# Optimization experiments

Measured on AMD Instinct MI355X. Metric: run time of the kernel, lower is better.

## Reference

```python
import jax, jax.numpy as jnp
import numpy as np

D_MODEL = 1024
D_STATE = 16
D_CONV = 4
EXPAND = 2
NUM_LAYERS = 2
SEQ = 1024
BATCH = 2
D_INNER = EXPAND * D_MODEL          # 2048
DT_RANK = (D_MODEL + 15) // 16      # 64 (math.ceil(d_model/16))


def setup_inputs() -> dict:
    key = jax.random.key(0)
    ks = jax.random.split(key, 10)
    s = 0.02
    # A initialized as in mamba_ssm: A = repeat(arange(1, d_state+1), d_inner) -> A_log = log(A)
    A_log = jnp.log(jnp.broadcast_to(
        jnp.arange(1, D_STATE + 1, dtype=jnp.float32), (NUM_LAYERS, D_INNER, D_STATE)))
    return {
        "pe": jax.random.normal(ks[0], (SEQ, D_MODEL), jnp.float32) * s,
        "condition": jax.random.normal(ks[1], (BATCH, SEQ, D_MODEL), jnp.float32),
        "W_in": jax.random.normal(ks[2], (NUM_LAYERS, 2 * D_INNER, D_MODEL), jnp.float32) * s,
        "conv_w": jax.random.normal(ks[3], (NUM_LAYERS, D_INNER, D_CONV), jnp.float32) * s,
        "conv_b": jnp.zeros((NUM_LAYERS, D_INNER), jnp.float32),
        "W_x": jax.random.normal(ks[4], (NUM_LAYERS, DT_RANK + 2 * D_STATE, D_INNER), jnp.float32) * s,
        "W_dt": jax.random.normal(ks[5], (NUM_LAYERS, D_INNER, DT_RANK), jnp.float32) * s,
        "b_dt": jax.random.normal(ks[6], (NUM_LAYERS, D_INNER), jnp.float32) * s,
        "A_log": A_log,
        "Dp": jnp.ones((NUM_LAYERS, D_INNER), jnp.float32),
        "W_out": jax.random.normal(ks[7], (NUM_LAYERS, D_MODEL, D_INNER), jnp.float32) * s,
        "output_shape": BATCH,
    }


def _mamba_block(x, W_in, conv_w, conv_b, W_x, W_dt, b_dt, A_log, Dp, W_out):
    # x: [B, L, d_model]
    B, L, _ = x.shape
    xz = jnp.einsum('bld,ed->ble', x, W_in)          # [B, L, 2*d_inner]
    u, z = jnp.split(xz, 2, axis=-1)                 # each [B, L, d_inner]
    # causal depthwise conv1d (padding=d_conv-1, truncate to L)
    xp = jnp.pad(u, ((0, 0), (D_CONV - 1, 0), (0, 0)))
    xc = conv_b + sum(conv_w[:, k] * xp[:, k:k + L, :] for k in range(D_CONV))
    xc = jax.nn.silu(xc)                             # [B, L, d_inner]
    x_dbl = jnp.einsum('bld,ed->ble', xc, W_x)       # [B, L, dt_rank + 2*d_state]
    dt, Bm, Cm = jnp.split(x_dbl, [DT_RANK, DT_RANK + D_STATE], axis=-1)
    delta = jax.nn.softplus(jnp.einsum('blr,dr->bld', dt, W_dt) + b_dt)  # [B, L, d_inner]
    A = -jnp.exp(A_log)                              # [d_inner, d_state]

    def step(h, inputs):
        u_t, d_t, B_t, C_t = inputs                  # [B,di],[B,di],[B,ds],[B,ds]
        dA = jnp.exp(d_t[:, :, None] * A)            # [B, di, ds]
        h = dA * h + (d_t * u_t)[:, :, None] * B_t[:, None, :]
        y = jnp.einsum('bds,bs->bd', h, C_t)
        return h, y

    h0 = jnp.zeros((B, D_INNER, D_STATE), x.dtype)
    xs = (xc.transpose(1, 0, 2), delta.transpose(1, 0, 2),
          Bm.transpose(1, 0, 2), Cm.transpose(1, 0, 2))
    _, ys = jax.lax.scan(step, h0, xs)               # ys: [L, B, d_inner]
    y = ys.transpose(1, 0, 2) + xc * Dp
    out = y * jax.nn.silu(z)
    return jnp.einsum('bld,ed->ble', out, W_out)     # [B, L, d_model]


def reference(pe, condition, W_in, conv_w, conv_b, W_x, W_dt, b_dt, A_log, Dp, W_out, output_shape):
    # pe.repeat(B,1,1) + condition
    x = pe[None, :, :] + condition
    for i in range(NUM_LAYERS):
        x = _mamba_block(x, W_in[i], conv_w[i], conv_b[i], W_x[i],
                         W_dt[i], b_dt[i], A_log[i], Dp[i], W_out[i])
    return x
```

## Files before the change

### kernel.cpp

```cpp
#include <hip/hip_runtime.h>
#include <math.h>

#define D_MODEL 1024
#define D_INNER 2048
#define D_STATE 16
#define DT_RANK 64
#define SEQ 1024
#define BATCH 2
#define NLAYERS 2
#define ROWS (BATCH*SEQ)
#define XDIM 96
#define XZLD (2*D_INNER)

#define NC 32
#define CL 32
#define SDB 256

#define G2_ROWS 64
#define G2_KC 128
#define G2_BK 32
#define G2_KS (D_INNER / G2_KC)

typedef short bf16x8 __attribute__((ext_vector_type(8)));
typedef float f32x4  __attribute__((ext_vector_type(4)));

__device__ __forceinline__ unsigned short f2bf(float f) {
    union { float f; unsigned int u; } v; v.f = f;
    unsigned int u = v.u;
    return (unsigned short)((u + 0x7FFFu + ((u >> 16) & 1u)) >> 16);
}
__device__ __forceinline__ float bf2f(unsigned short u) {
    union { unsigned int i; float f; } v; v.i = ((unsigned int)u) << 16; return v.f;
}

__device__ __forceinline__ void gload_lds16(const void* g, void* s) {
    __builtin_amdgcn_global_load_lds((const __attribute__((address_space(1))) void*)g,
                                     (__attribute__((address_space(3))) void*)s, 16, 0, 0);
}

__global__ __launch_bounds__(256) void add_pe_kernel(const float* __restrict__ pe,
    const float* __restrict__ cond, float* __restrict__ X)
{
    int i = blockIdx.x * 256 + threadIdx.x;
    int total = ROWS * D_MODEL / 4;
    if (i >= total) return;
    int row  = i / (D_MODEL / 4);
    int l    = row & (SEQ - 1);
    int col4 = i - row * (D_MODEL / 4);
    float4 p = reinterpret_cast<const float4*>(pe)[l * (D_MODEL / 4) + col4];
    float4 c = reinterpret_cast<const float4*>(cond)[i];
    float4 r; r.x = p.x + c.x; r.y = p.y + c.y; r.z = p.z + c.z; r.w = p.w + c.w;
    reinterpret_cast<float4*>(X)[i] = r;
}

__global__ __launch_bounds__(256) void add_pe_bf(const float* __restrict__ pe,
    const float* __restrict__ cond, unsigned short* __restrict__ Xbf)
{
    int i = blockIdx.x * 256 + threadIdx.x;
    int total = ROWS * D_MODEL / 4;
    if (i >= total) return;
    int row  = i / (D_MODEL / 4);
    int l    = row & (SEQ - 1);
    int col4 = i - row * (D_MODEL / 4);
    float4 p = reinterpret_cast<const float4*>(pe)[l * (D_MODEL / 4) + col4];
    float4 c = reinterpret_cast<const float4*>(cond)[i];
    ushort4 o;
    o.x = f2bf(p.x + c.x); o.y = f2bf(p.y + c.y);
    o.z = f2bf(p.z + c.z); o.w = f2bf(p.w + c.w);
    reinterpret_cast<ushort4*>(Xbf)[i] = o;
}

__global__ __launch_bounds__(256) void conv_bf16_dense(const float* __restrict__ src,
    unsigned short* __restrict__ dst, int n4)
{
    int i = blockIdx.x * 256 + threadIdx.x;
    if (i >= n4) return;
    float4 v = reinterpret_cast<const float4*>(src)[i];
    ushort4 o; o.x = f2bf(v.x); o.y = f2bf(v.y); o.z = f2bf(v.z); o.w = f2bf(v.w);
    reinterpret_cast<ushort4*>(dst)[i] = o;
}

#define WN1 (NLAYERS * 2 * D_INNER * D_MODEL / 4)
#define WN2 (NLAYERS * D_MODEL * D_INNER / 4)
#define WN3 (NLAYERS * D_INNER * DT_RANK / 4)
__global__ __launch_bounds__(256) void conv_wall(const float* __restrict__ Win,
    const float* __restrict__ Wout, const float* __restrict__ Wdt,
    unsigned short* __restrict__ WINbf, unsigned short* __restrict__ WOUTbf,
    unsigned short* __restrict__ WDTbf)
{
    int i = blockIdx.x * 256 + threadIdx.x;
    const float* src; unsigned short* dst; int j;
    if (i < WN1)              { src = Win;  dst = WINbf;  j = i; }
    else if (i < WN1 + WN2)   { src = Wout; dst = WOUTbf; j = i - WN1; }
    else if (i < WN1+WN2+WN3) { src = Wdt;  dst = WDTbf;  j = i - WN1 - WN2; }
    else return;
    float4 v = reinterpret_cast<const float4*>(src)[j];
    ushort4 o; o.x = f2bf(v.x); o.y = f2bf(v.y); o.z = f2bf(v.z); o.w = f2bf(v.w);
    reinterpret_cast<ushort4*>(dst)[j] = o;
}

__global__ __launch_bounds__(256) void conv_bf16_strided(const float* __restrict__ src,
    int ld, int cols, unsigned short* __restrict__ dst, int total4)
{
    int i = blockIdx.x * 256 + threadIdx.x;
    if (i >= total4) return;
    int c4  = cols / 4;
    int row = i / c4;
    int col = (i - row * c4) * 4;
    float4 v = *reinterpret_cast<const float4*>(src + (size_t)row * ld + col);
    ushort4 o; o.x = f2bf(v.x); o.y = f2bf(v.y); o.z = f2bf(v.z); o.w = f2bf(v.w);
    *reinterpret_cast<ushort4*>(dst + (size_t)row * cols + col) = o;
}

__global__ __launch_bounds__(256) void conv_bf16_dtcols(const float* __restrict__ XDBL,
    unsigned short* __restrict__ dst)
{
    int i = blockIdx.x * 256 + threadIdx.x;
    if (i >= ROWS * DT_RANK / 4) return;
    int m  = i >> 4;
    int c4 = (i & 15) * 4;
    float4 v = *reinterpret_cast<const float4*>(XDBL + (size_t)m * XDIM + c4);
    ushort4 o; o.x = f2bf(v.x); o.y = f2bf(v.y); o.z = f2bf(v.z); o.w = f2bf(v.w);
    *reinterpret_cast<ushort4*>(dst + (size_t)m * DT_RANK + c4) = o;
}

#define GBM 128
#define GBN 128
#define GBK 64

#define GEMM_STAGE(Ap, Bp, lda, ldb, koff)                                      \
    _Pragma("unroll")                                                           \
    for (int i_ = 0; i_ < 4; ++i_) {                                            \
        int off_ = w * 4096 + i_ * 1024 + l * 16;                               \
        int row_ = off_ >> 7;                                                   \
        int col_ = (off_ & 127) >> 1;                                           \
        gload_lds16(Ap + (size_t)(m0 + row_) * (lda) + (koff) + col_,           \
                    (char*)As + w * 4096 + i_ * 1024);                          \
    }                                                                           \
    _Pragma("unroll")                                                           \
    for (int i_ = 0; i_ < 4; ++i_) {                                            \
        int off_ = w * 4096 + i_ * 1024 + l * 16;                               \
        int row_ = off_ >> 7;                                                   \
        int col_ = (off_ & 127) >> 1;                                           \
        gload_lds16(Bp + (size_t)(n0 + row_) * (ldb) + (koff) + col_,           \
                    (char*)Bs + w * 4096 + i_ * 1024);                          \
    }

#define GEMM_MFMA_STEP                                                          \
    _Pragma("unroll")                                                           \
    for (int kk = 0; kk < 2; ++kk) {                                            \
        bf16x8 af[4], bfr[4];                                                   \
        _Pragma("unroll")                                                       \
        for (int m = 0; m < 4; ++m)                                             \
            af[m] = *(const bf16x8*)&As[(wr * 64 + m * 16 + fr) * GBK + kk * 32 + fq * 8]; \
        _Pragma("unroll")                                                       \
        for (int n = 0; n < 4; ++n)                                             \
            bfr[n] = *(const bf16x8*)&Bs[(wc * 64 + n * 16 + fr) * GBK + kk * 32 + fq * 8]; \
        _Pragma("unroll")                                                       \
        for (int m = 0; m < 4; ++m)                                             \
            _Pragma("unroll")                                                   \
            for (int n = 0; n < 4; ++n)                                         \
                acc[m][n] = __builtin_amdgcn_mfma_f32_16x16x32_bf16(af[m], bfr[n], acc[m][n], 0, 0, 0); \
    }

__global__ __launch_bounds__(256) void gemm_bf16_nt(const unsigned short* __restrict__ A,
    const unsigned short* __restrict__ B, float* __restrict__ C,
    int M, int N, int K, int ldc, const float* __restrict__ bias, int epilogue)
{
    __shared__ unsigned short As[GBM * GBK];
    __shared__ unsigned short Bs[GBN * GBK];
    int tid = threadIdx.x;
    int w = tid >> 6, l = tid & 63;
    int wr = w >> 1, wc = w & 1;
    int m0 = blockIdx.y * GBM, n0 = blockIdx.x * GBN;

    f32x4 acc[4][4];
    #pragma unroll
    for (int m = 0; m < 4; ++m)
        #pragma unroll
        for (int n = 0; n < 4; ++n) acc[m][n] = (f32x4){0.f, 0.f, 0.f, 0.f};
    int fr = l & 15, fq = l >> 4;

    for (int k0 = 0; k0 < K; k0 += GBK) {
        GEMM_STAGE(A, B, K, K, k0)
        __syncthreads();
        GEMM_MFMA_STEP
        __syncthreads();
    }

    #pragma unroll
    for (int m = 0; m < 4; ++m)
        #pragma unroll
        for (int n = 0; n < 4; ++n) {
            int col = n0 + wc * 64 + n * 16 + fr;
            #pragma unroll
            for (int j = 0; j < 4; ++j) {
                int row = m0 + wr * 64 + m * 16 + fq * 4 + j;
                float v = acc[m][n][j];
                if (epilogue == 1) {
                    v += bias[col];
                    v = fmaxf(v, 0.f) + log1pf(__expf(-fabsf(v)));
                }
                C[(size_t)row * ldc + col] = v;
            }
        }
}

__global__ __launch_bounds__(256) void gemm_bf16_nt_bfout(const unsigned short* __restrict__ A,
    const unsigned short* __restrict__ B, unsigned short* __restrict__ C,
    int M, int N, int K, int ldc)
{
    __shared__ unsigned short As[GBM * GBK];
    __shared__ unsigned short Bs[GBN * GBK];
    int tid = threadIdx.x;
    int w = tid >> 6, l = tid & 63;
    int wr = w >> 1, wc = w & 1;
    int m0 = blockIdx.y * GBM, n0 = blockIdx.x * GBN;

    f32x4 acc[4][4];
    #pragma unroll
    for (int m = 0; m < 4; ++m)
        #pragma unroll
        for (int n = 0; n < 4; ++n) acc[m][n] = (f32x4){0.f, 0.f, 0.f, 0.f};
    int fr = l & 15, fq = l >> 4;

    for (int k0 = 0; k0 < K; k0 += GBK) {
        GEMM_STAGE(A, B, K, K, k0)
        __syncthreads();
        GEMM_MFMA_STEP
        __syncthreads();
    }

    #pragma unroll
    for (int m = 0; m < 4; ++m)
        #pragma unroll
        for (int n = 0; n < 4; ++n) {
            int col = n0 + wc * 64 + n * 16 + fr;
            #pragma unroll
            for (int j = 0; j < 4; ++j) {
                int row = m0 + wr * 64 + m * 16 + fq * 4 + j;
                C[(size_t)row * ldc + col] = f2bf(acc[m][n][j]);
            }
        }
}

__global__ __launch_bounds__(256) void gemm_bf16_sp_bfout(const unsigned short* __restrict__ A,
    const unsigned short* __restrict__ B, unsigned short* __restrict__ C,
    int M, int N, int K, int ldc, const float* __restrict__ bias)
{
    __shared__ unsigned short As[GBM * GBK];
    __shared__ unsigned short Bs[GBN * GBK];
    int tid = threadIdx.x;
    int w = tid >> 6, l = tid & 63;
    int wr = w >> 1, wc = w & 1;
    int m0 = blockIdx.y * GBM, n0 = blockIdx.x * GBN;

    f32x4 acc[4][4];
    #pragma unroll
    for (int m = 0; m < 4; ++m)
        #pragma unroll
        for (int n = 0; n < 4; ++n) acc[m][n] = (f32x4){0.f, 0.f, 0.f, 0.f};
    int fr = l & 15, fq = l >> 4;

    for (int k0 = 0; k0 < K; k0 += GBK) {
        GEMM_STAGE(A, B, K, K, k0)
        __syncthreads();
        GEMM_MFMA_STEP
        __syncthreads();
    }

    #pragma unroll
    for (int m = 0; m < 4; ++m)
        #pragma unroll
        for (int n = 0; n < 4; ++n) {
            int col = n0 + wc * 64 + n * 16 + fr;
            float bv = bias[col];
            #pragma unroll
            for (int j = 0; j < 4; ++j) {
                int row = m0 + wr * 64 + m * 16 + fq * 4 + j;
                float v = acc[m][n][j] + bv;
                v = fmaxf(v, 0.f) + log1pf(__expf(-fabsf(v)));
                C[(size_t)row * ldc + col] = f2bf(v);
            }
        }
}

__global__ __launch_bounds__(256) void gemm_bf16_nt_ks(const unsigned short* __restrict__ A, int lda,
    const unsigned short* __restrict__ B, int ldb, float* __restrict__ P,
    int M, int N, int Kper)
{
    __shared__ unsigned short As[GBM * GBK];
    __shared__ unsigned short Bs[GBN * GBK];
    int tid = threadIdx.x;
    int w = tid >> 6, l = tid & 63;
    int wr = w >> 1, wc = w & 1;
    int m0 = blockIdx.y * GBM, n0 = blockIdx.x * GBN;
    int koff = blockIdx.z * Kper;
    float* Pz = P + (size_t)blockIdx.z * M * N;

    f32x4 acc[4][4];
    #pragma unroll
    for (int m = 0; m < 4; ++m)
        #pragma unroll
        for (int n = 0; n < 4; ++n) acc[m][n] = (f32x4){0.f, 0.f, 0.f, 0.f};
    int fr = l & 15, fq = l >> 4;

    for (int k0 = 0; k0 < Kper; k0 += GBK) {
        GEMM_STAGE(A, B, lda, ldb, koff + k0)
        __syncthreads();
        GEMM_MFMA_STEP
        __syncthreads();
    }

    #pragma unroll
    for (int m = 0; m < 4; ++m)
        #pragma unroll
        for (int n = 0; n < 4; ++n) {
            int col = n0 + wc * 64 + n * 16 + fr;
            #pragma unroll
            for (int j = 0; j < 4; ++j) {
                int row = m0 + wr * 64 + m * 16 + fq * 4 + j;
                Pz[(size_t)row * N + col] = acc[m][n][j];
            }
        }
}

__global__ __launch_bounds__(256) void gemm4_reduce(const float* __restrict__ P,
    float* __restrict__ X, unsigned short* __restrict__ Xbf)
{
    int i = blockIdx.x * 256 + threadIdx.x;
    if (i >= ROWS * D_MODEL / 4) return;
    float4 a = reinterpret_cast<const float4*>(P)[i];
    float4 b = reinterpret_cast<const float4*>(P + (size_t)ROWS * D_MODEL)[i];
    float4 r; r.x = a.x + b.x; r.y = a.y + b.y; r.z = a.z + b.z; r.w = a.w + b.w;
    if (X) reinterpret_cast<float4*>(X)[i] = r;
    if (Xbf) {
        ushort4 o; o.x = f2bf(r.x); o.y = f2bf(r.y); o.z = f2bf(r.z); o.w = f2bf(r.w);
        reinterpret_cast<ushort4*>(Xbf)[i] = o;
    }
}

__global__ __launch_bounds__(256) void gemm2_fused(const unsigned short* __restrict__ XZbf,
    const float* __restrict__ cw, const float* __restrict__ cb,
    const float* __restrict__ B, unsigned short* __restrict__ XCbf,
    float* __restrict__ P)
{
    __shared__ float Axc[G2_KC][68];
    __shared__ float Bs[G2_BK][XDIM + 1];
    int tid = threadIdx.x;
    int m0 = blockIdx.x * G2_ROWS;
    int kc = blockIdx.y;
    int k0 = kc * G2_KC;

    {
        int d_loc = tid & 127;
        int d     = k0 + d_loc;
        int r0    = m0 + (tid >> 7) * 32;
        float4 wv = *(const float4*)(cw + (size_t)d * 4);
        float cbv = cb[d];
        int l0 = r0 & (SEQ - 1);
        float u3 = (l0 >= 3) ? bf2f(XZbf[(size_t)(r0 - 3) * XZLD + d]) : 0.f;
        float u2 = (l0 >= 2) ? bf2f(XZbf[(size_t)(r0 - 2) * XZLD + d]) : 0.f;
        float u1 = (l0 >= 1) ? bf2f(XZbf[(size_t)(r0 - 1) * XZLD + d]) : 0.f;
        int rl0 = r0 - m0;
        #pragma unroll 4
        for (int t = 0; t < 32; ++t) {
            float u0 = bf2f(XZbf[(size_t)(r0 + t) * XZLD + d]);
            float v = cbv + wv.x * u3 + wv.y * u2 + wv.z * u1 + wv.w * u0;
            v = v / (1.f + __expf(-v));
            Axc[d_loc][rl0 + t] = v;
            XCbf[(size_t)(r0 + t) * D_INNER + d] = f2bf(v);
            u3 = u2; u2 = u1; u1 = u0;
        }
    }
    __syncthreads();

    int rg = tid >> 4;
    int cg = tid & 15;
    float acc[4][6];
    #pragma unroll
    for (int i = 0; i < 4; ++i)
        #pragma unroll
        for (int j = 0; j < 6; ++j) acc[i][j] = 0.f;

    for (int kb = 0; kb < G2_KC; kb += G2_BK) {
        {
            #pragma unroll
            for (int i = 0; i < 3; ++i) {
                int idx = tid + i * 256;
                int col = idx >> 3;
                int kk  = (idx & 7) * 4;
                float4 v = *(const float4*)(B + (size_t)col * D_INNER + k0 + kb + kk);
                Bs[kk + 0][col] = v.x;
                Bs[kk + 1][col] = v.y;
                Bs[kk + 2][col] = v.z;
                Bs[kk + 3][col] = v.w;
            }
        }
        __syncthreads();
        #pragma unroll
        for (int k = 0; k < G2_BK; ++k) {
            float4 a  = *(const float4*)&Axc[kb + k][rg * 4];
            float2 b0 = *(const float2*)&Bs[k][cg * 6];
            float2 b1 = *(const float2*)&Bs[k][cg * 6 + 2];
            float2 b2 = *(const float2*)&Bs[k][cg * 6 + 4];
            float av[4] = {a.x, a.y, a.z, a.w};
            float bv[6] = {b0.x, b0.y, b1.x, b1.y, b2.x, b2.y};
            #pragma unroll
            for (int i = 0; i < 4; ++i)
                #pragma unroll
                for (int j = 0; j < 6; ++j) acc[i][j] += av[i] * bv[j];
        }
        __syncthreads();
    }

    #pragma unroll
    for (int i = 0; i < 4; ++i)
        #pragma unroll
        for (int j = 0; j < 6; ++j)
            P[((size_t)kc * ROWS + m0 + rg * 4 + i) * XDIM + cg * 6 + j] = acc[i][j];
}

__global__ __launch_bounds__(256) void gemm2_splitk(const float* __restrict__ A,
    const float* __restrict__ B, float* __restrict__ P)
{
    __shared__ float As[G2_BK][G2_ROWS];
    __shared__ float Bs[G2_BK][XDIM + 1];
    int tid = threadIdx.x;
    int m0 = blockIdx.x * G2_ROWS;
    int kc = blockIdx.y;
    int k0 = kc * G2_KC;

    int rg = tid >> 4;
    int cg = tid & 15;
    float acc[4][6];
    #pragma unroll
    for (int i = 0; i < 4; ++i)
        #pragma unroll
        for (int j = 0; j < 6; ++j) acc[i][j] = 0.f;

    for (int kb = 0; kb < G2_KC; kb += G2_BK) {
        {
            int row = tid & 63;
            int kk  = (tid >> 6) * 4;
            #pragma unroll
            for (int i = 0; i < 2; ++i) {
                float4 v = *(const float4*)(A + (size_t)(m0 + row) * D_INNER + k0 + kb + kk + i * 16);
                As[kk + i * 16 + 0][row] = v.x;
                As[kk + i * 16 + 1][row] = v.y;
                As[kk + i * 16 + 2][row] = v.z;
                As[kk + i * 16 + 3][row] = v.w;
            }
        }
        {
            #pragma unroll
            for (int i = 0; i < 3; ++i) {
                int idx = tid + i * 256;
                int col = idx >> 3;
                int kk  = (idx & 7) * 4;
                float4 v = *(const float4*)(B + (size_t)col * D_INNER + k0 + kb + kk);
                Bs[kk + 0][col] = v.x;
                Bs[kk + 1][col] = v.y;
                Bs[kk + 2][col] = v.z;
                Bs[kk + 3][col] = v.w;
            }
        }
        __syncthreads();
        #pragma unroll
        for (int k = 0; k < G2_BK; ++k) {
            float4 a  = *(const float4*)&As[k][rg * 4];
            float2 b0 = *(const float2*)&Bs[k][cg * 6];
            float2 b1 = *(const float2*)&Bs[k][cg * 6 + 2];
            float2 b2 = *(const float2*)&Bs[k][cg * 6 + 4];
            float av[4] = {a.x, a.y, a.z, a.w};
            float bv[6] = {b0.x, b0.y, b1.x, b1.y, b2.x, b2.y};
            #pragma unroll
            for (int i = 0; i < 4; ++i)
                #pragma unroll
                for (int j = 0; j < 6; ++j) acc[i][j] += av[i] * bv[j];
        }
        __syncthreads();
    }

    #pragma unroll
    for (int i = 0; i < 4; ++i)
        #pragma unroll
        for (int j = 0; j < 6; ++j)
            P[((size_t)kc * ROWS + m0 + rg * 4 + i) * XDIM + cg * 6 + j] = acc[i][j];
}

__global__ __launch_bounds__(256) void gemm2_reduce(const float* __restrict__ P,
    float* __restrict__ XDBLo, unsigned short* __restrict__ dtbf)
{
    int i = blockIdx.x * 256 + threadIdx.x;
    if (i >= ROWS * XDIM / 4) return;
    float4 acc = make_float4(0.f, 0.f, 0.f, 0.f);
    #pragma unroll
    for (int ks = 0; ks < G2_KS; ++ks) {
        float4 v = *(const float4*)(P + (size_t)ks * ROWS * XDIM + (size_t)i * 4);
        acc.x += v.x; acc.y += v.y; acc.z += v.z; acc.w += v.w;
    }
    *(float4*)(XDBLo + (size_t)i * 4) = acc;
    if (dtbf) {
        int row = (i * 4) / XDIM;
        int col = (i * 4) - row * XDIM;
        if (col < DT_RANK) {
            ushort4 o; o.x = f2bf(acc.x); o.y = f2bf(acc.y); o.z = f2bf(acc.z); o.w = f2bf(acc.w);
            *reinterpret_cast<ushort4*>(dtbf + (size_t)row * DT_RANK + col) = o;
        }
    }
}

#define BM 64
#define BN 64
#define BK 16
__global__ __launch_bounds__(256) void gemm_nt(const float* __restrict__ A, int lda,
                                               const float* __restrict__ B, int ldb,
                                               float* __restrict__ C, int ldc,
                                               int M, int N, int K,
                                               const float* __restrict__ bias, int epilogue)
{
    __shared__ float As[BM][BK + 1];
    __shared__ float Bs[BN][BK + 1];
    int t  = threadIdx.x;
    int m0 = blockIdx.y * BM;
    int n0 = blockIdx.x * BN;
    int lrow = t >> 2;
    int lk   = (t & 3) * 4;
    int tm   = t >> 4;
    int tn   = t & 15;

    float acc[4][4];
    #pragma unroll
    for (int i = 0; i < 4; ++i)
        #pragma unroll
        for (int j = 0; j < 4; ++j) acc[i][j] = 0.f;

    for (int k0 = 0; k0 < K; k0 += BK) {
        {
            int row = m0 + lrow;
            float4 v = make_float4(0.f, 0.f, 0.f, 0.f);
            if (row < M) v = *reinterpret_cast<const float4*>(A + (size_t)row * lda + k0 + lk);
            As[lrow][lk + 0] = v.x; As[lrow][lk + 1] = v.y;
            As[lrow][lk + 2] = v.z; As[lrow][lk + 3] = v.w;
        }
        {
            int row = n0 + lrow;
            float4 v = make_float4(0.f, 0.f, 0.f, 0.f);
            if (row < N) v = *reinterpret_cast<const float4*>(B + (size_t)row * ldb + k0 + lk);
            Bs[lrow][lk + 0] = v.x; Bs[lrow][lk + 1] = v.y;
            Bs[lrow][lk + 2] = v.z; Bs[lrow][lk + 3] = v.w;
        }
        __syncthreads();
        #pragma unroll
        for (int kk = 0; kk < BK; ++kk) {
            float a[4], b[4];
            #pragma unroll
            for (int i = 0; i < 4; ++i) a[i] = As[tm * 4 + i][kk];
            #pragma unroll
            for (int j = 0; j < 4; ++j) b[j] = Bs[tn * 4 + j][kk];
            #pragma unroll
            for (int i = 0; i < 4; ++i)
                #pragma unroll
                for (int j = 0; j < 4; ++j) acc[i][j] += a[i] * b[j];
        }
        __syncthreads();
    }

    #pragma unroll
    for (int i = 0; i < 4; ++i) {
        int m = m0 + tm * 4 + i;
        if (m >= M) continue;
        #pragma unroll
        for (int j = 0; j < 4; ++j) {
            int n = n0 + tn * 4 + j;
            if (n >= N) continue;
            float v = acc[i][j];
            if (epilogue == 1) {
                v += bias[n];
                v = fmaxf(v, 0.f) + log1pf(__expf(-fabsf(v)));
            }
            C[(size_t)m * ldc + n] = v;
        }
    }
}

__global__ __launch_bounds__(256) void conv_silu_kernel(const float* __restrict__ XZ,
    const float* __restrict__ cw, const float* __restrict__ cb, float* __restrict__ XC)
{
    int idx = blockIdx.x * 256 + threadIdx.x;
    if (idx >= ROWS * (D_INNER / 4)) return;
    int d4   = idx % (D_INNER / 4);
    int rl   = idx / (D_INNER / 4);
    int l    = rl & (SEQ - 1);
    int base = rl - l;
    int d    = d4 * 4;

    float4 acc = reinterpret_cast<const float4*>(cb)[d4];
    float w[4][4];
    #pragma unroll
    for (int dd = 0; dd < 4; ++dd) {
        float4 wv = *reinterpret_cast<const float4*>(cw + (size_t)(d + dd) * 4);
        w[dd][0] = wv.x; w[dd][1] = wv.y; w[dd][2] = wv.z; w[dd][3] = wv.w;
    }
    #pragma unroll
    for (int k = 0; k < 4; ++k) {
        int lr = l - 3 + k;
        if (lr < 0) continue;
        float4 u = *reinterpret_cast<const float4*>(XZ + (size_t)(base + lr) * XZLD + d);
        acc.x += w[0][k] * u.x; acc.y += w[1][k] * u.y;
        acc.z += w[2][k] * u.z; acc.w += w[3][k] * u.w;
    }
    acc.x = acc.x / (1.f + __expf(-acc.x));
    acc.y = acc.y / (1.f + __expf(-acc.y));
    acc.z = acc.z / (1.f + __expf(-acc.z));
    acc.w = acc.w / (1.f + __expf(-acc.w));
    reinterpret_cast<float4*>(XC)[idx] = acc;
}


__global__ __launch_bounds__(SDB) void scan_part1b(const unsigned short* __restrict__ XCbf,
    const unsigned short* __restrict__ DL, const float* __restrict__ XDBL,
    const float* __restrict__ A_log, float* __restrict__ Psum, float* __restrict__ Ssum)
{
    __shared__ float sB[CL][16];
    int tid = threadIdx.x;
    int d = blockIdx.x * SDB + tid;
    int c = blockIdx.y, b = blockIdx.z;
    size_t r0 = (size_t)b * SEQ + (size_t)c * CL;

    if (tid < CL * 4) {
        int t = tid >> 2, j = (tid & 3) * 4;
        *(float4*)&sB[t][j] = *(const float4*)(XDBL + (r0 + t) * XDIM + DT_RANK + j);
    }

    float a[D_STATE], S[D_STATE];
    #pragma unroll
    for (int i = 0; i < 4; ++i) {
        float4 v = *(const float4*)(A_log + (size_t)d * D_STATE + i * 4);
        a[i*4+0] = -__expf(v.x); a[i*4+1] = -__expf(v.y);
        a[i*4+2] = -__expf(v.z); a[i*4+3] = -__expf(v.w);
    }
    #pragma unroll
    for (int s = 0; s < D_STATE; ++s) S[s] = 0.f;
    float sumdl = 0.f;
    __syncthreads();

    for (int t = 0; t < CL; ++t) {
        float dl = bf2f(DL[(r0 + t) * D_INNER + d]);
        float uu = bf2f(XCbf[(r0 + t) * D_INNER + d]);
        float du = dl * uu;
        sumdl += dl;
        float4 b0 = *(const float4*)&sB[t][0];
        float4 b1 = *(const float4*)&sB[t][4];
        float4 b2 = *(const float4*)&sB[t][8];
        float4 b3 = *(const float4*)&sB[t][12];
        float bv[16] = {b0.x,b0.y,b0.z,b0.w, b1.x,b1.y,b1.z,b1.w,
                        b2.x,b2.y,b2.z,b2.w, b3.x,b3.y,b3.z,b3.w};
        #pragma unroll
        for (int s = 0; s < D_STATE; ++s) {
            float e = __expf(dl * a[s]);
            S[s] = e * S[s] + du * bv[s];
        }
    }

    size_t o = (((size_t)b * NC + c) * D_INNER + d) * D_STATE;
    #pragma unroll
    for (int i = 0; i < 4; ++i) {
        float4 p, s4;
        p.x = __expf(a[i*4+0] * sumdl); p.y = __expf(a[i*4+1] * sumdl);
        p.z = __expf(a[i*4+2] * sumdl); p.w = __expf(a[i*4+3] * sumdl);
        s4.x = S[i*4+0]; s4.y = S[i*4+1]; s4.z = S[i*4+2]; s4.w = S[i*4+3];
        *(float4*)(Psum + o + i * 4) = p;
        *(float4*)(Ssum + o + i * 4) = s4;
    }
}

__global__ __launch_bounds__(256) void scan_prefix(float* __restrict__ Psum,
    const float* __restrict__ Ssum)
{
    int idx = blockIdx.x * 256 + threadIdx.x;
    int b = idx >> 15;
    int rem = idx & 32767;
    float h = 0.f;
    for (int c = 0; c < NC; ++c) {
        size_t o = (((size_t)b * NC + c) * D_INNER * D_STATE) + rem;
        float p = Psum[o];
        float s = Ssum[o];
        Psum[o] = h;
        h = p * h + s;
    }
}

__global__ __launch_bounds__(SDB) void scan_part2b(const unsigned short* __restrict__ XCbf,
    unsigned short* __restrict__ DL, const unsigned short* __restrict__ XZbf,
    const float* __restrict__ XDBL, const float* __restrict__ A_log,
    const float* __restrict__ Dp, const float* __restrict__ Hin)
{
    __shared__ float sBC[CL][32];
    int tid = threadIdx.x;
    int d = blockIdx.x * SDB + tid;
    int c = blockIdx.y, b = blockIdx.z;
    size_t r0 = (size_t)b * SEQ + (size_t)c * CL;

    {
        int t = tid >> 3, j = (tid & 7) * 4;
        *(float4*)&sBC[t][j] = *(const float4*)(XDBL + (r0 + t) * XDIM + DT_RANK + j);
    }

    float a[D_STATE], h[D_STATE];
    #pragma unroll
    for (int i = 0; i < 4; ++i) {
        float4 v = *(const float4*)(A_log + (size_t)d * D_STATE + i * 4);
        a[i*4+0] = -__expf(v.x); a[i*4+1] = -__expf(v.y);
        a[i*4+2] = -__expf(v.z); a[i*4+3] = -__expf(v.w);
    }
    size_t ho = (((size_t)b * NC + c) * D_INNER + d) * D_STATE;
    #pragma unroll
    for (int i = 0; i < 4; ++i) {
        float4 v = *(const float4*)(Hin + ho + i * 4);
        h[i*4+0] = v.x; h[i*4+1] = v.y; h[i*4+2] = v.z; h[i*4+3] = v.w;
    }
    float dp = Dp[d];
    __syncthreads();

    for (int t = 0; t < CL; ++t) {
        float dl = bf2f(DL[(r0 + t) * D_INNER + d]);
        float uu = bf2f(XCbf[(r0 + t) * D_INNER + d]);
        float z  = bf2f(XZbf[(r0 + t) * XZLD + D_INNER + d]);
        float du = dl * uu;
        float4 b0 = *(const float4*)&sBC[t][0];
        float4 b1 = *(const float4*)&sBC[t][4];
        float4 b2 = *(const float4*)&sBC[t][8];
        float4 b3 = *(const float4*)&sBC[t][12];
        float4 c0 = *(const float4*)&sBC[t][16];
        float4 c1 = *(const float4*)&sBC[t][20];
        float4 c2 = *(const float4*)&sBC[t][24];
        float4 c3 = *(const float4*)&sBC[t][28];
        float bv[16] = {b0.x,b0.y,b0.z,b0.w, b1.x,b1.y,b1.z,b1.w,
                        b2.x,b2.y,b2.z,b2.w, b3.x,b3.y,b3.z,b3.w};
        float cv[16] = {c0.x,c0.y,c0.z,c0.w, c1.x,c1.y,c1.z,c1.w,
                        c2.x,c2.y,c2.z,c2.w, c3.x,c3.y,c3.z,c3.w};
        float y = 0.f;
        #pragma unroll
        for (int s = 0; s < D_STATE; ++s) {
            float e = __expf(dl * a[s]);
            h[s] = e * h[s] + du * bv[s];
            y += h[s] * cv[s];
        }
        float sz = z / (1.f + __expf(-z));
        DL[(r0 + t) * D_INNER + d] = f2bf((y + uu * dp) * sz);
    }
}

__global__ __launch_bounds__(SDB) void scan_part1(const float* __restrict__ XC,
    const float* __restrict__ XZ, const float* __restrict__ XDBL,
    const float* __restrict__ A_log, float* __restrict__ Psum, float* __restrict__ Ssum)
{
    __shared__ float sB[CL][16];
    int tid = threadIdx.x;
    int d = blockIdx.x * SDB + tid;
    int c = blockIdx.y, b = blockIdx.z;
    size_t r0 = (size_t)b * SEQ + (size_t)c * CL;

    if (tid < CL * 4) {
        int t = tid >> 2, j = (tid & 3) * 4;
        *(float4*)&sB[t][j] = *(const float4*)(XDBL + (r0 + t) * XDIM + DT_RANK + j);
    }

    float a[D_STATE], S[D_STATE];
    #pragma unroll
    for (int i = 0; i < 4; ++i) {
        float4 v = *(const float4*)(A_log + (size_t)d * D_STATE + i * 4);
        a[i*4+0] = -__expf(v.x); a[i*4+1] = -__expf(v.y);
        a[i*4+2] = -__expf(v.z); a[i*4+3] = -__expf(v.w);
    }
    #pragma unroll
    for (int s = 0; s < D_STATE; ++s) S[s] = 0.f;
    float sumdl = 0.f;
    __syncthreads();

    for (int t = 0; t < CL; ++t) {
        float dl = XZ[(r0 + t) * XZLD + d];
        float uu = XC[(r0 + t) * D_INNER + d];
        float du = dl * uu;
        sumdl += dl;
        float4 b0 = *(const float4*)&sB[t][0];
        float4 b1 = *(const float4*)&sB[t][4];
        float4 b2 = *(const float4*)&sB[t][8];
        float4 b3 = *(const float4*)&sB[t][12];
        float bv[16] = {b0.x,b0.y,b0.z,b0.w, b1.x,b1.y,b1.z,b1.w,
                        b2.x,b2.y,b2.z,b2.w, b3.x,b3.y,b3.z,b3.w};
        #pragma unroll
        for (int s = 0; s < D_STATE; ++s) {
            float e = __expf(dl * a[s]);
            S[s] = e * S[s] + du * bv[s];
        }
    }

    size_t o = (((size_t)b * NC + c) * D_INNER + d) * D_STATE;
    #pragma unroll
    for (int i = 0; i < 4; ++i) {
        float4 p, s4;
        p.x = __expf(a[i*4+0] * sumdl); p.y = __expf(a[i*4+1] * sumdl);
        p.z = __expf(a[i*4+2] * sumdl); p.w = __expf(a[i*4+3] * sumdl);
        s4.x = S[i*4+0]; s4.y = S[i*4+1]; s4.z = S[i*4+2]; s4.w = S[i*4+3];
        *(float4*)(Psum + o + i * 4) = p;
        *(float4*)(Ssum + o + i * 4) = s4;
    }
}

__global__ __launch_bounds__(SDB) void scan_part2(const float* __restrict__ XC,
    float* __restrict__ XZ, const float* __restrict__ XDBL,
    const float* __restrict__ A_log, const float* __restrict__ Dp,
    const float* __restrict__ Hin)
{
    __shared__ float sBC[CL][32];
    int tid = threadIdx.x;
    int d = blockIdx.x * SDB + tid;
    int c = blockIdx.y, b = blockIdx.z;
    size_t r0 = (size_t)b * SEQ + (size_t)c * CL;

    {
        int t = tid >> 3, j = (tid & 7) * 4;
        *(float4*)&sBC[t][j] = *(const float4*)(XDBL + (r0 + t) * XDIM + DT_RANK + j);
    }

    float a[D_STATE], h[D_STATE];
    #pragma unroll
    for (int i = 0; i < 4; ++i) {
        float4 v = *(const float4*)(A_log + (size_t)d * D_STATE + i * 4);
        a[i*4+0] = -__expf(v.x); a[i*4+1] = -__expf(v.y);
        a[i*4+2] = -__expf(v.z); a[i*4+3] = -__expf(v.w);
    }
    size_t ho = (((size_t)b * NC + c) * D_INNER + d) * D_STATE;
    #pragma unroll
    for (int i = 0; i < 4; ++i) {
        float4 v = *(const float4*)(Hin + ho + i * 4);
        h[i*4+0] = v.x; h[i*4+1] = v.y; h[i*4+2] = v.z; h[i*4+3] = v.w;
    }
    float dp = Dp[d];
    __syncthreads();

    for (int t = 0; t < CL; ++t) {
        float dl = XZ[(r0 + t) * XZLD + d];
        float uu = XC[(r0 + t) * D_INNER + d];
        float z  = XZ[(r0 + t) * XZLD + D_INNER + d];
        float du = dl * uu;
        float4 b0 = *(const float4*)&sBC[t][0];
        float4 b1 = *(const float4*)&sBC[t][4];
        float4 b2 = *(const float4*)&sBC[t][8];
        float4 b3 = *(const float4*)&sBC[t][12];
        float4 c0 = *(const float4*)&sBC[t][16];
        float4 c1 = *(const float4*)&sBC[t][20];
        float4 c2 = *(const float4*)&sBC[t][24];
        float4 c3 = *(const float4*)&sBC[t][28];
        float bv[16] = {b0.x,b0.y,b0.z,b0.w, b1.x,b1.y,b1.z,b1.w,
                        b2.x,b2.y,b2.z,b2.w, b3.x,b3.y,b3.z,b3.w};
        float cv[16] = {c0.x,c0.y,c0.z,c0.w, c1.x,c1.y,c1.z,c1.w,
                        c2.x,c2.y,c2.z,c2.w, c3.x,c3.y,c3.z,c3.w};
        float y = 0.f;
        #pragma unroll
        for (int s = 0; s < D_STATE; ++s) {
            float e = __expf(dl * a[s]);
            h[s] = e * h[s] + du * bv[s];
            y += h[s] * cv[s];
        }
        float sz = z / (1.f + __expf(-z));
        XZ[(r0 + t) * XZLD + d] = (y + uu * dp) * sz;
    }
}

__global__ __launch_bounds__(256) void scan_kernel2(const float* __restrict__ XC,
    float* __restrict__ XZ, const float* __restrict__ XDBL,
    const float* __restrict__ A_log, const float* __restrict__ Dp)
{
    int tid = threadIdx.x;
    int s  = tid & 15;
    int dd = tid >> 4;
    int d  = blockIdx.x * 16 + dd;
    int b  = blockIdx.y;

    float a  = -__expf(A_log[(size_t)d * D_STATE + s]);
    float h  = 0.f;
    float dp = Dp[d];
    const size_t rbase = (size_t)b * SEQ;

    for (int t = 0; t < SEQ; ++t) {
        size_t r = rbase + t;
        float dl = XZ[r * XZLD + d];
        float uu = XC[r * D_INNER + d];
        float z  = XZ[r * XZLD + D_INNER + d];
        float Bv = XDBL[r * XDIM + DT_RANK + s];
        float Cv = XDBL[r * XDIM + DT_RANK + D_STATE + s];
        float e  = __expf(dl * a);
        h = e * h + dl * uu * Bv;
        float y = h * Cv;
        y += __shfl_xor(y, 1);
        y += __shfl_xor(y, 2);
        y += __shfl_xor(y, 4);
        y += __shfl_xor(y, 8);
        if (s == 0) {
            float sz = z / (1.f + __expf(-z));
            XZ[r * XZLD + d] = (y + uu * dp) * sz;
        }
    }
}

extern "C" void kernel_launch(void* const* d_in, const int* in_sizes, int n_in,
                              void* d_out, int out_size, void* d_ws, size_t ws_size,
                              hipStream_t stream)
{
    const float* pe    = (const float*)d_in[0];
    const float* cond  = (const float*)d_in[1];
    const float* W_in  = (const float*)d_in[2];
    const float* cw    = (const float*)d_in[3];
    const float* cb    = (const float*)d_in[4];
    const float* W_x   = (const float*)d_in[5];
    const float* W_dt  = (const float*)d_in[6];
    const float* b_dt  = (const float*)d_in[7];
    const float* A_log = (const float*)d_in[8];
    const float* Dp    = (const float*)d_in[9];
    const float* W_out = (const float*)d_in[10];

    float* X = (float*)d_out;

    char* wsp = (char*)d_ws;
    unsigned short* XZbf = (unsigned short*)wsp;
    unsigned short* XCbf = (unsigned short*)(wsp + 16777216);
    float* XDBL  = (float*)(wsp + 33554432);
    unsigned short* BF0   = (unsigned short*)(wsp + 34340864);
    unsigned short* dtbf  = (unsigned short*)(wsp + 42729472);
    unsigned short* WINbf = (unsigned short*)(wsp + 42991616);
    unsigned short* WOUTbf= (unsigned short*)(wsp + 59768832);
    unsigned short* WDTbf = (unsigned short*)(wsp + 68157440);
    float* SCR   = (float*)(wsp + 68681728);
    size_t need_A = 68681728 + 16777216;

    float* XZb   = (float*)d_ws;
    float* XCb   = XZb + (size_t)ROWS * XZLD;
    float* XDBLb = XCb + (size_t)ROWS * D_INNER;
    void* rest = (void*)(XDBLb + (size_t)ROWS * XDIM);
    unsigned short* Abf = (unsigned short*)rest;
    unsigned short* Bbf = Abf + (size_t)ROWS * D_INNER;
    float* PpartB = (float*)rest;
    float* PsumB  = (float*)rest;
    float* SsumB  = PsumB + (size_t)BATCH * NC * D_INNER * D_STATE;
    size_t need_B = ((size_t)ROWS * XZLD + (size_t)ROWS * D_INNER + (size_t)ROWS * XDIM) * 4
                  + ((size_t)ROWS * D_INNER + (size_t)ROWS * D_INNER) * 2;

    if (ws_size >= need_A) {
        float* Psum = SCR;
        float* Ssum = SCR + (size_t)BATCH * NC * D_INNER * D_STATE;

        conv_wall<<<(WN1 + WN2 + WN3 + 255) / 256, 256, 0, stream>>>(
            W_in, W_out, W_dt, WINbf, WOUTbf, WDTbf);
        add_pe_bf<<<ROWS * D_MODEL / 4 / 256, 256, 0, stream>>>(pe, cond, BF0);

        for (int l = 0; l < NLAYERS; ++l) {
            const unsigned short* WINl  = WINbf  + (size_t)l * 2 * D_INNER * D_MODEL;
            const unsigned short* WOUTl = WOUTbf + (size_t)l * D_MODEL * D_INNER;
            const unsigned short* WDTl  = WDTbf  + (size_t)l * D_INNER * DT_RANK;
            const float* W_x_l   = W_x   + (size_t)l * XDIM * D_INNER;
            const float* b_dt_l  = b_dt  + (size_t)l * D_INNER;
            const float* A_log_l = A_log + (size_t)l * D_INNER * D_STATE;
            const float* Dp_l    = Dp    + (size_t)l * D_INNER;

            gemm_bf16_nt_bfout<<<dim3(2 * D_INNER / GBN, ROWS / GBM), 256, 0, stream>>>(
                BF0, WINl, XZbf, ROWS, 2 * D_INNER, D_MODEL, XZLD);
            gemm2_fused<<<dim3(ROWS / G2_ROWS, G2_KS), 256, 0, stream>>>(
                XZbf, cw + (size_t)l * D_INNER * 4, cb + (size_t)l * D_INNER,
                W_x_l, XCbf, SCR);
            gemm2_reduce<<<(ROWS * XDIM / 4 + 255) / 256, 256, 0, stream>>>(SCR, XDBL, dtbf);
            gemm_bf16_sp_bfout<<<dim3(D_INNER / GBN, ROWS / GBM), 256, 0, stream>>>(
                dtbf, WDTl, BF0, ROWS, D_INNER, DT_RANK, D_INNER, b_dt_l);
            scan_part1b<<<dim3(D_INNER / SDB, NC, BATCH), SDB, 0, stream>>>(
                XCbf, BF0, XDBL, A_log_l, Psum, Ssum);
            scan_prefix<<<BATCH * D_INNER * D_STATE / 256, 256, 0, stream>>>(Psum, Ssum);
            scan_part2b<<<dim3(D_INNER / SDB, NC, BATCH), SDB, 0, stream>>>(
                XCbf, BF0, XZbf, XDBL, A_log_l, Dp_l, Psum);
            gemm_bf16_nt_ks<<<dim3(D_MODEL / GBN, ROWS / GBM, 2), 256, 0, stream>>>(
                BF0, D_INNER, WOUTl, D_INNER, SCR, ROWS, D_MODEL, D_INNER / 2);
            gemm4_reduce<<<(ROWS * D_MODEL / 4 + 255) / 256, 256, 0, stream>>>(
                SCR, (l == NLAYERS - 1) ? X : nullptr, (l < NLAYERS - 1) ? BF0 : nullptr);
        }
    } else if (ws_size >= need_B) {
        add_pe_kernel<<<ROWS * D_MODEL / 4 / 256, 256, 0, stream>>>(pe, cond, X);
        for (int l = 0; l < NLAYERS; ++l) {
            const float* W_in_l  = W_in  + (size_t)l * 2 * D_INNER * D_MODEL;
            const float* W_out_l = W_out + (size_t)l * D_MODEL * D_INNER;
            const float* W_x_l   = W_x   + (size_t)l * XDIM * D_INNER;
            const float* W_dt_l  = W_dt  + (size_t)l * D_INNER * DT_RANK;
            const float* b_dt_l  = b_dt  + (size_t)l * D_INNER;
            const float* A_log_l = A_log + (size_t)l * D_INNER * D_STATE;
            const float* Dp_l    = Dp    + (size_t)l * D_INNER;

            conv_bf16_dense<<<(ROWS * D_MODEL / 4 + 255) / 256, 256, 0, stream>>>(X, Abf, ROWS * D_MODEL / 4);
            conv_bf16_dense<<<(2 * D_INNER * D_MODEL / 4 + 255) / 256, 256, 0, stream>>>(W_in_l, Bbf, 2 * D_INNER * D_MODEL / 4);
            gemm_bf16_nt<<<dim3(2 * D_INNER / GBN, ROWS / GBM), 256, 0, stream>>>(
                Abf, Bbf, XZb, ROWS, 2 * D_INNER, D_MODEL, XZLD, nullptr, 0);
            conv_silu_kernel<<<ROWS * (D_INNER / 4) / 256, 256, 0, stream>>>(
                XZb, cw + (size_t)l * D_INNER * 4, cb + (size_t)l * D_INNER, XCb);
            gemm2_splitk<<<dim3(ROWS / G2_ROWS, G2_KS), 256, 0, stream>>>(XCb, W_x_l, PpartB);
            gemm2_reduce<<<(ROWS * XDIM / 4 + 255) / 256, 256, 0, stream>>>(PpartB, XDBLb, nullptr);
            conv_bf16_dtcols<<<(ROWS * DT_RANK / 4 + 255) / 256, 256, 0, stream>>>(XDBLb, Abf);
            conv_bf16_dense<<<(D_INNER * DT_RANK / 4 + 255) / 256, 256, 0, stream>>>(W_dt_l, Bbf, D_INNER * DT_RANK / 4);
            gemm_bf16_nt<<<dim3(D_INNER / GBN, ROWS / GBM), 256, 0, stream>>>(
                Abf, Bbf, XZb, ROWS, D_INNER, DT_RANK, XZLD, b_dt_l, 1);
            scan_part1<<<dim3(D_INNER / SDB, NC, BATCH), SDB, 0, stream>>>(
                XCb, XZb, XDBLb, A_log_l, PsumB, SsumB);
            scan_prefix<<<BATCH * D_INNER * D_STATE / 256, 256, 0, stream>>>(PsumB, SsumB);
            scan_part2<<<dim3(D_INNER / SDB, NC, BATCH), SDB, 0, stream>>>(
                XCb, XZb, XDBLb, A_log_l, Dp_l, PsumB);
            conv_bf16_strided<<<(ROWS * D_INNER / 4 + 255) / 256, 256, 0, stream>>>(
                XZb, XZLD, D_INNER, Abf, ROWS * D_INNER / 4);
            conv_bf16_dense<<<(D_MODEL * D_INNER / 4 + 255) / 256, 256, 0, stream>>>(W_out_l, Bbf, D_MODEL * D_INNER / 4);
            gemm_bf16_nt<<<dim3(D_MODEL / GBN, ROWS / GBM), 256, 0, stream>>>(
                Abf, Bbf, X, ROWS, D_MODEL, D_INNER, D_MODEL, nullptr, 0);
        }
    } else {
        add_pe_kernel<<<ROWS * D_MODEL / 4 / 256, 256, 0, stream>>>(pe, cond, X);
        for (int l = 0; l < NLAYERS; ++l) {
            gemm_nt<<<dim3(2 * D_INNER / BN, ROWS / BM), 256, 0, stream>>>(
                X, D_MODEL, W_in + (size_t)l * 2 * D_INNER * D_MODEL, D_MODEL,
                XZb, XZLD, ROWS, 2 * D_INNER, D_MODEL, nullptr, 0);
            conv_silu_kernel<<<ROWS * (D_INNER / 4) / 256, 256, 0, stream>>>(
                XZb, cw + (size_t)l * D_INNER * 4, cb + (size_t)l * D_INNER, XCb);
            gemm_nt<<<dim3((XDIM + BN - 1) / BN, ROWS / BM), 256, 0, stream>>>(
                XCb, D_INNER, W_x + (size_t)l * XDIM * D_INNER, D_INNER,
                XDBLb, XDIM, ROWS, XDIM, D_INNER, nullptr, 0);
            gemm_nt<<<dim3(D_INNER / BN, ROWS / BM), 256, 0, stream>>>(
                XDBLb, XDIM, W_dt + (size_t)l * D_INNER * DT_RANK, DT_RANK,
                XZb, XZLD, ROWS, D_INNER, DT_RANK, b_dt + (size_t)l * D_INNER, 1);
            scan_kernel2<<<dim3(D_INNER / 16, BATCH), 256, 0, stream>>>(
                XCb, XZb, XDBLb, A_log + (size_t)l * D_INNER * D_STATE, Dp + (size_t)l * D_INNER);
            gemm_nt<<<dim3(D_MODEL / BN, ROWS / BM), 256, 0, stream>>>(
                XZb, XZLD, W_out + (size_t)l * D_MODEL * D_INNER, D_INNER,
                X, D_MODEL, ROWS, D_MODEL, D_INNER, nullptr, 0);
        }
    }
}
```

Before: 342.6 us.

## Recompute causal conv+SiLU inside scan kernels instead of storing XC buffer

Drops the bf16 XC intermediate written by the fused conv/x_proj kernel. Both scan passes now recompute the depthwise conv and SiLU from the XZ buffer with a rolling window, reading the three previous rows at chunk boundaries. The add-pe kernel is also merged into the weight-conversion launch, saving one launch. This trades a 8 MB write and two reads for extra exp and FMA work in each scan pass, where accumulated rounding may differ slightly.

```diff
diff --git a/kernel.cpp b/kernel.cpp
--- a/kernel.cpp
+++ b/kernel.cpp
@@ -53,23 +53,6 @@
     reinterpret_cast<float4*>(X)[i] = r;
 }
 
-__global__ __launch_bounds__(256) void add_pe_bf(const float* __restrict__ pe,
-    const float* __restrict__ cond, unsigned short* __restrict__ Xbf)
-{
-    int i = blockIdx.x * 256 + threadIdx.x;
-    int total = ROWS * D_MODEL / 4;
-    if (i >= total) return;
-    int row  = i / (D_MODEL / 4);
-    int l    = row & (SEQ - 1);
-    int col4 = i - row * (D_MODEL / 4);
-    float4 p = reinterpret_cast<const float4*>(pe)[l * (D_MODEL / 4) + col4];
-    float4 c = reinterpret_cast<const float4*>(cond)[i];
-    ushort4 o;
-    o.x = f2bf(p.x + c.x); o.y = f2bf(p.y + c.y);
-    o.z = f2bf(p.z + c.z); o.w = f2bf(p.w + c.w);
-    reinterpret_cast<ushort4*>(Xbf)[i] = o;
-}
-
 __global__ __launch_bounds__(256) void conv_bf16_dense(const float* __restrict__ src,
     unsigned short* __restrict__ dst, int n4)
 {
@@ -83,20 +66,40 @@
 #define WN1 (NLAYERS * 2 * D_INNER * D_MODEL / 4)
 #define WN2 (NLAYERS * D_MODEL * D_INNER / 4)
 #define WN3 (NLAYERS * D_INNER * DT_RANK / 4)
+#define WN4 (ROWS * D_MODEL / 4)
 __global__ __launch_bounds__(256) void conv_wall(const float* __restrict__ Win,
     const float* __restrict__ Wout, const float* __restrict__ Wdt,
+    const float* __restrict__ pe, const float* __restrict__ cond,
     unsigned short* __restrict__ WINbf, unsigned short* __restrict__ WOUTbf,
-    unsigned short* __restrict__ WDTbf)
+    unsigned short* __restrict__ WDTbf, unsigned short* __restrict__ Xbf)
 {
     int i = blockIdx.x * 256 + threadIdx.x;
-    const float* src; unsigned short* dst; int j;
-    if (i < WN1)              { src = Win;  dst = WINbf;  j = i; }
-    else if (i < WN1 + WN2)   { src = Wout; dst = WOUTbf; j = i - WN1; }
-    else if (i < WN1+WN2+WN3) { src = Wdt;  dst = WDTbf;  j = i - WN1 - WN2; }
-    else return;
-    float4 v = reinterpret_cast<const float4*>(src)[j];
-    ushort4 o; o.x = f2bf(v.x); o.y = f2bf(v.y); o.z = f2bf(v.z); o.w = f2bf(v.w);
-    reinterpret_cast<ushort4*>(dst)[j] = o;
+    if (i < WN1) {
+        float4 v = reinterpret_cast<const float4*>(Win)[i];
+        ushort4 o; o.x = f2bf(v.x); o.y = f2bf(v.y); o.z = f2bf(v.z); o.w = f2bf(v.w);
+        reinterpret_cast<ushort4*>(WINbf)[i] = o;
+    } else if (i < WN1 + WN2) {
+        int j = i - WN1;
+        float4 v = reinterpret_cast<const float4*>(Wout)[j];
+        ushort4 o; o.x = f2bf(v.x); o.y = f2bf(v.y); o.z = f2bf(v.z); o.w = f2bf(v.w);
+        reinterpret_cast<ushort4*>(WOUTbf)[j] = o;
+    } else if (i < WN1 + WN2 + WN3) {
+        int j = i - WN1 - WN2;
+        float4 v = reinterpret_cast<const float4*>(Wdt)[j];
+        ushort4 o; o.x = f2bf(v.x); o.y = f2bf(v.y); o.z = f2bf(v.z); o.w = f2bf(v.w);
+        reinterpret_cast<ushort4*>(WDTbf)[j] = o;
+    } else if (i < WN1 + WN2 + WN3 + WN4) {
+        int j = i - WN1 - WN2 - WN3;
+        int row  = j / (D_MODEL / 4);
+        int l    = row & (SEQ - 1);
+        int col4 = j - row * (D_MODEL / 4);
+        float4 p = reinterpret_cast<const float4*>(pe)[l * (D_MODEL / 4) + col4];
+        float4 c = reinterpret_cast<const float4*>(cond)[j];
+        ushort4 o;
+        o.x = f2bf(p.x + c.x); o.y = f2bf(p.y + c.y);
+        o.z = f2bf(p.z + c.z); o.w = f2bf(p.w + c.w);
+        reinterpret_cast<ushort4*>(Xbf)[j] = o;
+    }
 }
 
 __global__ __launch_bounds__(256) void conv_bf16_strided(const float* __restrict__ src,
@@ -342,8 +345,7 @@
 
 __global__ __launch_bounds__(256) void gemm2_fused(const unsigned short* __restrict__ XZbf,
     const float* __restrict__ cw, const float* __restrict__ cb,
-    const float* __restrict__ B, unsigned short* __restrict__ XCbf,
-    float* __restrict__ P)
+    const float* __restrict__ B, float* __restrict__ P)
 {
     __shared__ float Axc[G2_KC][68];
     __shared__ float Bs[G2_BK][XDIM + 1];
@@ -369,7 +371,6 @@
             float v = cbv + wv.x * u3 + wv.y * u2 + wv.z * u1 + wv.w * u0;
             v = v / (1.f + __expf(-v));
             Axc[d_loc][rl0 + t] = v;
-            XCbf[(size_t)(r0 + t) * D_INNER + d] = f2bf(v);
             u3 = u2; u2 = u1; u1 = u0;
         }
     }
@@ -619,9 +620,26 @@
 }
 
 
-__global__ __launch_bounds__(SDB) void scan_part1b(const unsigned short* __restrict__ XCbf,
+#define XC_ROLL_INIT                                                            \
+    float4 wv = *(const float4*)(cw + (size_t)d * 4);                           \
+    float cbv = cb[d];                                                          \
+    float u3 = 0.f, u2 = 0.f, u1 = 0.f;                                         \
+    if (c > 0) {                                                                \
+        u3 = bf2f(XZbf[(r0 - 3) * XZLD + d]);                                   \
+        u2 = bf2f(XZbf[(r0 - 2) * XZLD + d]);                                   \
+        u1 = bf2f(XZbf[(r0 - 1) * XZLD + d]);                                   \
+    }
+
+#define XC_ROLL_STEP(uu_out)                                                    \
+    float u0 = bf2f(XZbf[(r0 + t) * XZLD + d]);                                 \
+    float cv_ = cbv + wv.x * u3 + wv.y * u2 + wv.z * u1 + wv.w * u0;            \
+    float uu_out = cv_ / (1.f + __expf(-cv_));                                  \
+    u3 = u2; u2 = u1; u1 = u0;
+
+__global__ __launch_bounds__(SDB) void scan_part1c(const unsigned short* __restrict__ XZbf,
     const unsigned short* __restrict__ DL, const float* __restrict__ XDBL,
-    const float* __restrict__ A_log, float* __restrict__ Psum, float* __restrict__ Ssum)
+    const float* __restrict__ A_log, const float* __restrict__ cw,
+    const float* __restrict__ cb, float* __restrict__ Psum, float* __restrict__ Ssum)
 {
     __shared__ float sB[CL][16];
     int tid = threadIdx.x;
@@ -644,11 +662,12 @@
     #pragma unroll
     for (int s = 0; s < D_STATE; ++s) S[s] = 0.f;
     float sumdl = 0.f;
+    XC_ROLL_INIT
     __syncthreads();
 
     for (int t = 0; t < CL; ++t) {
         float dl = bf2f(DL[(r0 + t) * D_INNER + d]);
-        float uu = bf2f(XCbf[(r0 + t) * D_INNER + d]);
+        XC_ROLL_STEP(uu)
         float du = dl * uu;
         sumdl += dl;
         float4 b0 = *(const float4*)&sB[t][0];
@@ -692,10 +711,11 @@
     }
 }
 
-__global__ __launch_bounds__(SDB) void scan_part2b(const unsigned short* __restrict__ XCbf,
-    unsigned short* __restrict__ DL, const unsigned short* __restrict__ XZbf,
-    const float* __restrict__ XDBL, const float* __restrict__ A_log,
-    const float* __restrict__ Dp, const float* __restrict__ Hin)
+__global__ __launch_bounds__(SDB) void scan_part2c(const unsigned short* __restrict__ XZbf,
+    unsigned short* __restrict__ DL, const float* __restrict__ XDBL,
+    const float* __restrict__ A_log, const float* __restrict__ cw,
+    const float* __restrict__ cb, const float* __restrict__ Dp,
+    const float* __restrict__ Hin)
 {
     __shared__ float sBC[CL][32];
     int tid = threadIdx.x;
@@ -722,12 +742,13 @@
         h[i*4+0] = v.x; h[i*4+1] = v.y; h[i*4+2] = v.z; h[i*4+3] = v.w;
     }
     float dp = Dp[d];
+    XC_ROLL_INIT
     __syncthreads();
 
     for (int t = 0; t < CL; ++t) {
         float dl = bf2f(DL[(r0 + t) * D_INNER + d]);
-        float uu = bf2f(XCbf[(r0 + t) * D_INNER + d]);
         float z  = bf2f(XZbf[(r0 + t) * XZLD + D_INNER + d]);
+        XC_ROLL_STEP(uu)
         float du = dl * uu;
         float4 b0 = *(const float4*)&sBC[t][0];
         float4 b1 = *(const float4*)&sBC[t][4];
@@ -927,7 +948,6 @@
 
     char* wsp = (char*)d_ws;
     unsigned short* XZbf = (unsigned short*)wsp;
-    unsigned short* XCbf = (unsigned short*)(wsp + 16777216);
     float* XDBL  = (float*)(wsp + 33554432);
     unsigned short* BF0   = (unsigned short*)(wsp + 34340864);
     unsigned short* dtbf  = (unsigned short*)(wsp + 42729472);
@@ -953,15 +973,16 @@
         float* Psum = SCR;
         float* Ssum = SCR + (size_t)BATCH * NC * D_INNER * D_STATE;
 
-        conv_wall<<<(WN1 + WN2 + WN3 + 255) / 256, 256, 0, stream>>>(
-            W_in, W_out, W_dt, WINbf, WOUTbf, WDTbf);
-        add_pe_bf<<<ROWS * D_MODEL / 4 / 256, 256, 0, stream>>>(pe, cond, BF0);
+        conv_wall<<<(WN1 + WN2 + WN3 + WN4 + 255) / 256, 256, 0, stream>>>(
+            W_in, W_out, W_dt, pe, cond, WINbf, WOUTbf, WDTbf, BF0);
 
         for (int l = 0; l < NLAYERS; ++l) {
             const unsigned short* WINl  = WINbf  + (size_t)l * 2 * D_INNER * D_MODEL;
             const unsigned short* WOUTl = WOUTbf + (size_t)l * D_MODEL * D_INNER;
             const unsigned short* WDTl  = WDTbf  + (size_t)l * D_INNER * DT_RANK;
             const float* W_x_l   = W_x   + (size_t)l * XDIM * D_INNER;
+            const float* cw_l    = cw    + (size_t)l * D_INNER * 4;
+            const float* cb_l    = cb    + (size_t)l * D_INNER;
             const float* b_dt_l  = b_dt  + (size_t)l * D_INNER;
             const float* A_log_l = A_log + (size_t)l * D_INNER * D_STATE;
             const float* Dp_l    = Dp    + (size_t)l * D_INNER;
@@ -969,16 +990,15 @@
             gemm_bf16_nt_bfout<<<dim3(2 * D_INNER / GBN, ROWS / GBM), 256, 0, stream>>>(
                 BF0, WINl, XZbf, ROWS, 2 * D_INNER, D_MODEL, XZLD);
             gemm2_fused<<<dim3(ROWS / G2_ROWS, G2_KS), 256, 0, stream>>>(
-                XZbf, cw + (size_t)l * D_INNER * 4, cb + (size_t)l * D_INNER,
-                W_x_l, XCbf, SCR);
+                XZbf, cw_l, cb_l, W_x_l, SCR);
             gemm2_reduce<<<(ROWS * XDIM / 4 + 255) / 256, 256, 0, stream>>>(SCR, XDBL, dtbf);
             gemm_bf16_sp_bfout<<<dim3(D_INNER / GBN, ROWS / GBM), 256, 0, stream>>>(
                 dtbf, WDTl, BF0, ROWS, D_INNER, DT_RANK, D_INNER, b_dt_l);
-            scan_part1b<<<dim3(D_INNER / SDB, NC, BATCH), SDB, 0, stream>>>(
-                XCbf, BF0, XDBL, A_log_l, Psum, Ssum);
+            scan_part1c<<<dim3(D_INNER / SDB, NC, BATCH), SDB, 0, stream>>>(
+                XZbf, BF0, XDBL, A_log_l, cw_l, cb_l, Psum, Ssum);
             scan_prefix<<<BATCH * D_INNER * D_STATE / 256, 256, 0, stream>>>(Psum, Ssum);
-            scan_part2b<<<dim3(D_INNER / SDB, NC, BATCH), SDB, 0, stream>>>(
-                XCbf, BF0, XZbf, XDBL, A_log_l, Dp_l, Psum);
+            scan_part2c<<<dim3(D_INNER / SDB, NC, BATCH), SDB, 0, stream>>>(
+                XZbf, BF0, XDBL, A_log_l, cw_l, cb_l, Dp_l, Psum);
             gemm_bf16_nt_ks<<<dim3(D_MODEL / GBN, ROWS / GBM, 2), 256, 0, stream>>>(
                 BF0, D_INNER, WOUTl, D_INNER, SCR, ROWS, D_MODEL, D_INNER / 2);
             gemm4_reduce<<<(ROWS * D_MODEL / 4 + 255) / 256, 256, 0, stream>>>(
```

Result: slower. 362.6 us (+5.8%).
